# Performance work log

Measured on AMD Instinct MI355X. Metric: run time of the kernel, lower is better.

## Reference

```python
import jax, jax.numpy as jnp
import numpy as np

N_NODES = 100000
N_EDGES = 1600000
IN_DIM = 128
HID = 64


def _init_linear(key, fan_in, fan_out):
    kw, kb = jax.random.split(key)
    bound = 1.0 / np.sqrt(fan_in)
    W = jax.random.uniform(kw, (fan_in, fan_out), jnp.float32, -bound, bound)
    b = jax.random.uniform(kb, (fan_out,), jnp.float32, -bound, bound)
    return W, b


def setup_inputs() -> dict:
    key = jax.random.key(0)
    ks = jax.random.split(key, 6)
    x = jax.random.normal(ks[0], (N_NODES, IN_DIM), jnp.float32)
    edge_index = jax.random.randint(ks[1], (2, N_EDGES), 0, N_NODES, jnp.int64)
    W_pre, b_pre = _init_linear(ks[2], IN_DIM, HID)
    W1, b1 = _init_linear(ks[3], HID, HID)
    W2, b2 = _init_linear(ks[4], HID, HID)
    W3, b3 = _init_linear(ks[5], HID, HID)
    return {"x": x, "edge_index": edge_index, "W_pre": W_pre, "b_pre": b_pre,
            "W1": W1, "b1": b1, "W2": W2, "b2": b2, "W3": W3, "b3": b3}


def _gcn_layer(h, src, dst, dinv, W, b):
    # PyG GCNConv: h' = D^{-1/2} (A + I) D^{-1/2} (h W) + b, deg from A+I
    n = h.shape[0]
    hw = h @ W                                  # [N, out]
    norm = dinv[src] * dinv[dst]                # [E]
    msg = hw[src] * norm[:, None]               # gather + scale  [E, out]
    agg = jax.ops.segment_sum(msg, dst, num_segments=n)  # scatter-add
    agg = agg + hw * (dinv * dinv)[:, None]     # self-loop term (norm = dinv_i^2)
    return agg + b


def reference(x, edge_index, W_pre, b_pre, W1, b1, W2, b2, W3, b3):
    src, dst = edge_index[0], edge_index[1]
    n = x.shape[0]
    # degree of A + I (self loops added, as in GCNConv default)
    deg = jax.ops.segment_sum(jnp.ones(src.shape[0], x.dtype), dst, num_segments=n) + 1.0
    dinv = jax.lax.rsqrt(deg)

    h = x @ W_pre + b_pre                       # feature_pre linear
    h = jax.nn.relu(_gcn_layer(h, src, dst, dinv, W1, b1))  # dropout is identity in eval
    h = jax.nn.relu(_gcn_layer(h, src, dst, dinv, W2, b2))
    h = _gcn_layer(h, src, dst, dinv, W3, b3)
    # F.normalize(p=2, dim=-1) with eps=1e-12
    nrm = jnp.linalg.norm(h, axis=-1, keepdims=True)
    return h / jnp.maximum(nrm, 1e-12)
```

## Files before the change

kernel.cpp:

```cpp
#include <hip/hip_runtime.h>

#define N_NODES 100000
#define N_EDGES 1600000
#define IN_DIM 128
#define HID 64
#define NB 782
#define NBLK_GEMM 782
#define NGROUP 25000

typedef __attribute__((ext_vector_type(8))) _Float16 h8v;
typedef __attribute__((ext_vector_type(4))) float f4v;

struct Args {
  const float* x; const int* ei;
  const float* Wp; const float* bp;
  const float* W1; const float* b1;
  const float* W2; const float* b2;
  const float* W3; const float* b3;
  float* out;
  _Float16* bufA16; _Float16* hw16;
  int* pairs; int* csr; int* offs; float* dinv;
  int* bsz; int* bboff; int* bcur;
  _Float16* WpH; _Float16* WpL; _Float16* W1H; _Float16* W1L;
  _Float16* W2H; _Float16* W2L; _Float16* W3H; _Float16* W3L;
};

__device__ __forceinline__ void d_split(const float* __restrict__ W,
                                        _Float16* __restrict__ hi,
                                        _Float16* __restrict__ lo, int K, int i) {
  int k = i >> 6, n = i & 63;
  float v = W[i];
  _Float16 h = (_Float16)v;
  float r = v - (float)h;
  hi[n * K + k] = h;
  lo[n * K + k] = (_Float16)r;
}

__global__ __launch_bounds__(256) void f_prep(Args a) {
  int blk = blockIdx.x, t = threadIdx.x;
  if (blk < 32) d_split(a.Wp, a.WpH, a.WpL, IN_DIM, blk * 256 + t);
  else if (blk < 48) d_split(a.W1, a.W1H, a.W1L, HID, (blk - 32) * 256 + t);
  else if (blk < 64) d_split(a.W2, a.W2H, a.W2L, HID, (blk - 48) * 256 + t);
  else d_split(a.W3, a.W3H, a.W3L, HID, (blk - 64) * 256 + t);
}

__global__ __launch_bounds__(256) void f_bhist(Args a) {
  __shared__ int cnt[NB];
  int t = threadIdx.x;
  for (int i = t; i < NB; i += 256) cnt[i] = 0;
  __syncthreads();
  int e0 = blockIdx.x * 8192, e1 = min(e0 + 8192, N_EDGES);
  for (int e = e0 + t; e < e1; e += 256)
    atomicAdd(&cnt[a.ei[N_EDGES + e] >> 7], 1);
  __syncthreads();
  for (int i = t; i < NB; i += 256)
    if (cnt[i]) atomicAdd(&a.bsz[i], cnt[i]);
}

__global__ __launch_bounds__(256) void f_bscan(Args a) {
  __shared__ int sm[256];
  int t = threadIdx.x;
  int c[4];
  int idx0 = t * 4;
#pragma unroll
  for (int j = 0; j < 4; ++j) c[j] = (idx0 + j < NB) ? a.bsz[idx0 + j] : 0;
  int tsum = c[0] + c[1] + c[2] + c[3];
  int val = tsum;
  sm[t] = val;
  __syncthreads();
  for (int off = 1; off < 256; off <<= 1) {
    int u = (t >= off) ? sm[t - off] : 0;
    __syncthreads();
    val += u;
    sm[t] = val;
    __syncthreads();
  }
  int excl = val - tsum;
#pragma unroll
  for (int j = 0; j < 4; ++j) {
    int idx = idx0 + j;
    if (idx < NB) { a.bboff[idx] = excl; a.bcur[idx] = excl; }
    excl += c[j];
  }
  if (t == 255) a.bboff[NB] = val;
}

__global__ __launch_bounds__(256) void f_partition(Args a) {
  __shared__ int cnt[NB];
  __shared__ int base[NB];
  int t = threadIdx.x;
  for (int i = t; i < NB; i += 256) cnt[i] = 0;
  __syncthreads();
  int e0 = blockIdx.x * 8192, e1 = min(e0 + 8192, N_EDGES);
  for (int e = e0 + t; e < e1; e += 256)
    atomicAdd(&cnt[a.ei[N_EDGES + e] >> 7], 1);
  __syncthreads();
  for (int i = t; i < NB; i += 256) {
    int c = cnt[i];
    base[i] = c ? atomicAdd(&a.bcur[i], c) : 0;
    cnt[i] = 0;
  }
  __syncthreads();
  for (int e = e0 + t; e < e1; e += 256) {
    int s = a.ei[e];
    int d = a.ei[N_EDGES + e];
    int b = d >> 7;
    int r = atomicAdd(&cnt[b], 1);
    a.pairs[base[b] + r] = ((d & 127) << 17) | s;
  }
}

__global__ __launch_bounds__(256) void f_csrdeg(Args a) {
  __shared__ int ldeg[128];
  __shared__ int sc[128];
  __shared__ int lcur[128];
  int t = threadIdx.x;
  int b = blockIdx.x;
  int node0 = b << 7;
  int nloc = min(128, N_NODES - node0);
  int beg = a.bboff[b], end = a.bboff[b + 1];
  if (t < 128) ldeg[t] = 0;
  __syncthreads();
  for (int i = beg + t; i < end; i += 256)
    atomicAdd(&ldeg[(a.pairs[i] >> 17) & 127], 1);
  __syncthreads();
  int dv = (t < 128) ? ldeg[t] : 0;
  if (t < 128) sc[t] = dv;
  __syncthreads();
  for (int off = 1; off < 128; off <<= 1) {
    int u = (t >= off && t < 128) ? sc[t - off] : 0;
    __syncthreads();
    if (t < 128) sc[t] += u;
    __syncthreads();
  }
  if (t < nloc) {
    int o = beg + sc[t] - dv;
    a.offs[node0 + t] = o;
    lcur[t] = o;
    a.dinv[node0 + t] = rsqrtf((float)dv + 1.0f);
  }
  if (b == NB - 1 && t == 0) a.offs[N_NODES] = N_EDGES;
  __syncthreads();
  for (int i = beg + t; i < end; i += 256) {
    int p = a.pairs[i];
    int pos = atomicAdd(&lcur[(p >> 17) & 127], 1);
    a.csr[pos] = p & 131071;
  }
}

__global__ __launch_bounds__(256) void f_gemm_pre(Args a) {
  __shared__ _Float16 sW[2 * 64 * IN_DIM];
  int t = threadIdx.x;
  int wave = t >> 6, lane = t & 63, fi = lane & 15, quad = lane >> 4;
  int r0 = blockIdx.x * 128 + wave * 32;

  f4v xb0[8], xb1[8];
  {
    int row = r0 + fi; if (row >= N_NODES) row = N_NODES - 1;
    const float* xp = a.x + (size_t)row * IN_DIM + quad * 8;
#pragma unroll
    for (int j = 0; j < 4; ++j) {
      xb0[2 * j]     = *(const f4v*)(xp + j * 32);
      xb0[2 * j + 1] = *(const f4v*)(xp + j * 32 + 4);
    }
  }
#pragma unroll
  for (int i = 0; i < 8; ++i) {
    int c = i * 256 + t;
    int h = c >> 10;
    int c2 = c & 1023;
    int n = c2 >> 4;
    const _Float16* src = (h ? a.WpL : a.WpH) + c2 * 8;
    f4v v = *(const f4v*)src;
    int off = (h << 14) | ((c2 * 16) ^ ((n & 7) << 4));
    *(f4v*)((char*)sW + off) = v;
  }
  __syncthreads();

  float bv[4];
#pragma unroll
  for (int ct = 0; ct < 4; ++ct) bv[ct] = a.bp[ct * 16 + fi];

#pragma unroll
  for (int f = 0; f < 2; ++f) {
    f4v* xcur = (f & 1) ? xb1 : xb0;
    f4v* xnxt = (f & 1) ? xb0 : xb1;
    if (f < 1) {
      int row = r0 + 16 + fi; if (row >= N_NODES) row = N_NODES - 1;
      const float* xp = a.x + (size_t)row * IN_DIM + quad * 8;
#pragma unroll
      for (int j = 0; j < 4; ++j) {
        xnxt[2 * j]     = *(const f4v*)(xp + j * 32);
        xnxt[2 * j + 1] = *(const f4v*)(xp + j * 32 + 4);
      }
    }
    f4v acc[4];
#pragma unroll
    for (int ct = 0; ct < 4; ++ct) acc[ct] = (f4v){0.f, 0.f, 0.f, 0.f};
#pragma unroll
    for (int k0i = 0; k0i < 4; ++k0i) {
      h8v ah, al;
#pragma unroll
      for (int j = 0; j < 4; ++j) {
        float v0 = xcur[2 * k0i][j], v1 = xcur[2 * k0i + 1][j];
        _Float16 h0 = (_Float16)v0, h1 = (_Float16)v1;
        ah[j] = h0;     al[j] = (_Float16)(v0 - (float)h0);
        ah[4 + j] = h1; al[4 + j] = (_Float16)(v1 - (float)h1);
      }
#pragma unroll
      for (int ct = 0; ct < 4; ++ct) {
        int n = ct * 16 + fi;
        int bo = ((n * IN_DIM + k0i * 32 + quad * 8) * 2) ^ ((n & 7) << 4);
        h8v bh = *(const h8v*)((const char*)sW + bo);
        h8v bl = *(const h8v*)((const char*)sW + 16384 + bo);
        acc[ct] = __builtin_amdgcn_mfma_f32_16x16x32_f16(ah, bh, acc[ct], 0, 0, 0);
        acc[ct] = __builtin_amdgcn_mfma_f32_16x16x32_f16(al, bh, acc[ct], 0, 0, 0);
        acc[ct] = __builtin_amdgcn_mfma_f32_16x16x32_f16(ah, bl, acc[ct], 0, 0, 0);
      }
    }
    int ro = r0 + f * 16;
#pragma unroll
    for (int ct = 0; ct < 4; ++ct) {
#pragma unroll
      for (int j = 0; j < 4; ++j) {
        int orow = ro + quad * 4 + j;
        if (orow < N_NODES)
          a.bufA16[(size_t)orow * HID + ct * 16 + fi] = (_Float16)(acc[ct][j] + bv[ct]);
      }
    }
  }
}

__global__ __launch_bounds__(256) void f_gemm64(Args a, const _Float16* __restrict__ Wh,
                                                const _Float16* __restrict__ Wl) {
  int t = threadIdx.x;
  int wave = t >> 6, lane = t & 63, fi = lane & 15, quad = lane >> 4;
  int r0 = blockIdx.x * 128 + wave * 32;

  h8v a0[2], a1[2];
  {
    int row = r0 + fi; if (row >= N_NODES) row = N_NODES - 1;
    const _Float16* xp = a.bufA16 + (size_t)row * HID + quad * 8;
    a0[0] = *(const h8v*)xp;
    a0[1] = *(const h8v*)(xp + 32);
  }
  h8v Bh[2][4], Bl[2][4];
#pragma unroll
  for (int k0i = 0; k0i < 2; ++k0i)
#pragma unroll
    for (int ct = 0; ct < 4; ++ct) {
      size_t o = (size_t)(ct * 16 + fi) * HID + k0i * 32 + quad * 8;
      Bh[k0i][ct] = *(const h8v*)(Wh + o);
      Bl[k0i][ct] = *(const h8v*)(Wl + o);
    }

#pragma unroll
  for (int f = 0; f < 2; ++f) {
    h8v* av = (f & 1) ? a1 : a0;
    h8v* nx = (f & 1) ? a0 : a1;
    if (f < 1) {
      int row = r0 + 16 + fi; if (row >= N_NODES) row = N_NODES - 1;
      const _Float16* xp = a.bufA16 + (size_t)row * HID + quad * 8;
      nx[0] = *(const h8v*)xp;
      nx[1] = *(const h8v*)(xp + 32);
    }
    f4v acc[4];
#pragma unroll
    for (int ct = 0; ct < 4; ++ct) acc[ct] = (f4v){0.f, 0.f, 0.f, 0.f};
#pragma unroll
    for (int k0i = 0; k0i < 2; ++k0i)
#pragma unroll
      for (int ct = 0; ct < 4; ++ct) {
        acc[ct] = __builtin_amdgcn_mfma_f32_16x16x32_f16(av[k0i], Bh[k0i][ct], acc[ct], 0, 0, 0);
        acc[ct] = __builtin_amdgcn_mfma_f32_16x16x32_f16(av[k0i], Bl[k0i][ct], acc[ct], 0, 0, 0);
      }
    int ro = r0 + f * 16;
#pragma unroll
    for (int ct = 0; ct < 4; ++ct)
#pragma unroll
      for (int j = 0; j < 4; ++j) {
        int orow = ro + quad * 4 + j;
        if (orow < N_NODES)
          a.hw16[(size_t)orow * HID + ct * 16 + fi] = (_Float16)acc[ct][j];
      }
  }
}

template <int MODE>
__device__ __forceinline__ void d_agg(int grp, const _Float16* __restrict__ hw,
                                      const int* __restrict__ offs,
                                      const int* __restrict__ csr,
                                      const float* __restrict__ dinv,
                                      const float* __restrict__ bias,
                                      _Float16* __restrict__ out16,
                                      float* __restrict__ out32) {
  int node = grp * 4 + (threadIdx.x >> 6);
  int lane = threadIdx.x & 63;
  int oct = lane >> 3;
  int fi = lane & 7;
  float di = dinv[node];
  int beg = offs[node];
  int end = offs[node + 1];

  float acc[8];
#pragma unroll
  for (int c = 0; c < 8; ++c) acc[c] = 0.f;

  if (oct == 0) {
    h8v hv = *(const h8v*)(hw + (size_t)node * HID + fi * 8);
    float w = di * di;
#pragma unroll
    for (int c = 0; c < 8; ++c) acc[c] += (float)hv[c] * w;
  }
  for (int e0 = beg + oct; e0 < end; e0 += 32) {
    int ss[4];
    float ww[4];
#pragma unroll
    for (int j = 0; j < 4; ++j) {
      int e = e0 + 8 * j;
      bool v = e < end;
      int s = csr[v ? e : beg];
      ss[j] = v ? s : node;
      ww[j] = v ? di : 0.0f;
    }
#pragma unroll
    for (int j = 0; j < 4; ++j) ww[j] *= dinv[ss[j]];
    h8v hv[4];
#pragma unroll
    for (int j = 0; j < 4; ++j)
      hv[j] = *(const h8v*)(hw + (size_t)ss[j] * HID + fi * 8);
#pragma unroll
    for (int j = 0; j < 4; ++j)
#pragma unroll
      for (int c = 0; c < 8; ++c) acc[c] += (float)hv[j][c] * ww[j];
  }
#pragma unroll
  for (int c = 0; c < 8; ++c) {
    float v = acc[c];
    v += __shfl_xor(v, 8);
    v += __shfl_xor(v, 16);
    v += __shfl_xor(v, 32);
    acc[c] = v;
  }
  if (oct == 0) {
#pragma unroll
    for (int c = 0; c < 8; ++c) acc[c] += bias[fi * 8 + c];
    if (MODE == 0) {
      h8v o;
#pragma unroll
      for (int c = 0; c < 8; ++c) o[c] = (_Float16)fmaxf(acc[c], 0.f);
      *(h8v*)(out16 + (size_t)node * HID + fi * 8) = o;
    } else {
      float ss = 0.f;
#pragma unroll
      for (int c = 0; c < 8; ++c) ss += acc[c] * acc[c];
      ss += __shfl_xor(ss, 1);
      ss += __shfl_xor(ss, 2);
      ss += __shfl_xor(ss, 4);
      float sc = 1.0f / fmaxf(sqrtf(ss), 1e-12f);
      f4v o0 = {acc[0] * sc, acc[1] * sc, acc[2] * sc, acc[3] * sc};
      f4v o1 = {acc[4] * sc, acc[5] * sc, acc[6] * sc, acc[7] * sc};
      *(f4v*)(out32 + (size_t)node * HID + fi * 8) = o0;
      *(f4v*)(out32 + (size_t)node * HID + fi * 8 + 4) = o1;
    }
  }
}

__global__ __launch_bounds__(256) void f_agg_relu(Args a, const float* bias) {
  d_agg<0>(blockIdx.x, a.hw16, a.offs, a.csr, a.dinv, bias, a.bufA16, nullptr);
}

__global__ __launch_bounds__(256) void f_agg_norm(Args a) {
  d_agg<1>(blockIdx.x, a.hw16, a.offs, a.csr, a.dinv, a.b3, nullptr, a.out);
}

extern "C" void kernel_launch(void* const* d_in, const int* in_sizes, int n_in,
                              void* d_out, int out_size, void* d_ws, size_t ws_size,
                              hipStream_t stream) {
  char* ws = (char*)d_ws;
  Args a;
  a.x  = (const float*)d_in[0];
  a.ei = (const int*)d_in[1];
  a.Wp = (const float*)d_in[2];  a.bp = (const float*)d_in[3];
  a.W1 = (const float*)d_in[4];  a.b1 = (const float*)d_in[5];
  a.W2 = (const float*)d_in[6];  a.b2 = (const float*)d_in[7];
  a.W3 = (const float*)d_in[8];  a.b3 = (const float*)d_in[9];
  a.out  = (float*)d_out;
  a.bufA16 = (_Float16*)(ws + 0);
  a.hw16   = (_Float16*)(ws + 12800000);
  a.pairs  = (int*)(ws + 25600000);
  a.csr    = (int*)(ws + 32000000);
  a.offs   = (int*)(ws + 38400000);
  a.dinv   = (float*)(ws + 38800016);
  a.bsz    = (int*)(ws + 39200016);
  a.bboff  = (int*)(ws + 39203152);
  a.bcur   = (int*)(ws + 39206288);
  a.WpH = (_Float16*)(ws + 39210000);
  a.WpL = (_Float16*)(ws + 39226384);
  a.W1H = (_Float16*)(ws + 39242768);
  a.W1L = (_Float16*)(ws + 39250960);
  a.W2H = (_Float16*)(ws + 39259152);
  a.W2L = (_Float16*)(ws + 39267344);
  a.W3H = (_Float16*)(ws + 39275536);
  a.W3L = (_Float16*)(ws + 39283728);

  (void)hipMemsetAsync(a.bsz, 0, NB * sizeof(int), stream);
  f_prep<<<80, 256, 0, stream>>>(a);
  f_bhist<<<196, 256, 0, stream>>>(a);
  f_bscan<<<1, 256, 0, stream>>>(a);
  f_partition<<<196, 256, 0, stream>>>(a);
  f_csrdeg<<<NB, 256, 0, stream>>>(a);
  f_gemm_pre<<<NBLK_GEMM, 256, 0, stream>>>(a);
  f_gemm64<<<NBLK_GEMM, 256, 0, stream>>>(a, a.W1H, a.W1L);
  f_agg_relu<<<NGROUP, 256, 0, stream>>>(a, a.b1);
  f_gemm64<<<NBLK_GEMM, 256, 0, stream>>>(a, a.W2H, a.W2L);
  f_agg_relu<<<NGROUP, 256, 0, stream>>>(a, a.b2);
  f_gemm64<<<NBLK_GEMM, 256, 0, stream>>>(a, a.W3H, a.W3L);
  f_agg_norm<<<NGROUP, 256, 0, stream>>>(a);
}
```

Measured before the change: 347.3 us.

## Restructure GCN aggregation to one feature per lane with readlane-broadcast neighbors

Replaces the 8-octet-by-8-feature aggregation (each octet handles separate edges with 16-byte fp16 vector loads, then a cross-octet shuffle reduction) with a scheme where each lane owns one feature. Edge indices and weights are loaded cooperatively 64 at a time and broadcast with readlane, so every lane gathers one fp16 element per neighbor. This removes the final shuffle reduction and the idle-octet writeback, but switches from 16-byte to 2-byte per-lane gather loads and serializes the edges of each node across iterations.

```diff
diff --git a/kernel.cpp b/kernel.cpp
--- a/kernel.cpp
+++ b/kernel.cpp
@@ -296,73 +296,46 @@
                                       float* __restrict__ out32) {
   int node = grp * 4 + (threadIdx.x >> 6);
   int lane = threadIdx.x & 63;
-  int oct = lane >> 3;
-  int fi = lane & 7;
   float di = dinv[node];
   int beg = offs[node];
   int end = offs[node + 1];
-
-  float acc[8];
-#pragma unroll
-  for (int c = 0; c < 8; ++c) acc[c] = 0.f;
-
-  if (oct == 0) {
-    h8v hv = *(const h8v*)(hw + (size_t)node * HID + fi * 8);
-    float w = di * di;
-#pragma unroll
-    for (int c = 0; c < 8; ++c) acc[c] += (float)hv[c] * w;
-  }
-  for (int e0 = beg + oct; e0 < end; e0 += 32) {
-    int ss[4];
-    float ww[4];
-#pragma unroll
-    for (int j = 0; j < 4; ++j) {
-      int e = e0 + 8 * j;
-      bool v = e < end;
-      int s = csr[v ? e : beg];
-      ss[j] = v ? s : node;
-      ww[j] = v ? di : 0.0f;
-    }
-#pragma unroll
-    for (int j = 0; j < 4; ++j) ww[j] *= dinv[ss[j]];
-    h8v hv[4];
-#pragma unroll
-    for (int j = 0; j < 4; ++j)
-      hv[j] = *(const h8v*)(hw + (size_t)ss[j] * HID + fi * 8);
-#pragma unroll
-    for (int j = 0; j < 4; ++j)
-#pragma unroll
-      for (int c = 0; c < 8; ++c) acc[c] += (float)hv[j][c] * ww[j];
-  }
-#pragma unroll
-  for (int c = 0; c < 8; ++c) {
-    float v = acc[c];
-    v += __shfl_xor(v, 8);
-    v += __shfl_xor(v, 16);
-    v += __shfl_xor(v, 32);
-    acc[c] = v;
-  }
-  if (oct == 0) {
-#pragma unroll
-    for (int c = 0; c < 8; ++c) acc[c] += bias[fi * 8 + c];
-    if (MODE == 0) {
-      h8v o;
-#pragma unroll
-      for (int c = 0; c < 8; ++c) o[c] = (_Float16)fmaxf(acc[c], 0.f);
-      *(h8v*)(out16 + (size_t)node * HID + fi * 8) = o;
-    } else {
-      float ss = 0.f;
-#pragma unroll
-      for (int c = 0; c < 8; ++c) ss += acc[c] * acc[c];
-      ss += __shfl_xor(ss, 1);
-      ss += __shfl_xor(ss, 2);
-      ss += __shfl_xor(ss, 4);
-      float sc = 1.0f / fmaxf(sqrtf(ss), 1e-12f);
-      f4v o0 = {acc[0] * sc, acc[1] * sc, acc[2] * sc, acc[3] * sc};
-      f4v o1 = {acc[4] * sc, acc[5] * sc, acc[6] * sc, acc[7] * sc};
-      *(f4v*)(out32 + (size_t)node * HID + fi * 8) = o0;
-      *(f4v*)(out32 + (size_t)node * HID + fi * 8 + 4) = o1;
-    }
+  int deg = end - beg;
+  float bv = bias[lane];
+
+  _Float16 hself = hw[(size_t)node * HID + lane];
+  float acc = (float)hself * (di * di);
+
+  for (int c0 = 0; c0 < deg; c0 += 64) {
+    int nc = min(64, deg - c0);
+    int ei = beg + c0 + ((lane < nc) ? lane : (nc - 1));
+    int sv = csr[ei];
+    float wv = (lane < nc) ? dinv[sv] * di : 0.0f;
+
+    int rn = (nc + 7) & ~7;
+    for (int j = 0; j < rn; j += 8) {
+      _Float16 v[8];
+      float wj[8];
+#pragma unroll
+      for (int u = 0; u < 8; ++u) {
+        int sj = __builtin_amdgcn_readlane(sv, j + u);
+        wj[u] = __int_as_float(__builtin_amdgcn_readlane(__float_as_int(wv), j + u));
+        const _Float16* p = hw + ((size_t)sj << 6);
+        v[u] = p[lane];
+      }
+#pragma unroll
+      for (int u = 0; u < 8; ++u) acc += (float)v[u] * wj[u];
+    }
+  }
+
+  acc += bv;
+  if (MODE == 0) {
+    out16[(size_t)node * HID + lane] = (_Float16)fmaxf(acc, 0.f);
+  } else {
+    float ss = acc * acc;
+#pragma unroll
+    for (int w = 1; w < 64; w <<= 1) ss += __shfl_xor(ss, w);
+    float sc = 1.0f / fmaxf(sqrtf(ss), 1e-12f);
+    out32[(size_t)node * HID + lane] = acc * sc;
   }
 }
 
```

Measured after the change: 358.8 us. 1.03x slower.

## Pre-scale CSR indices to byte offsets and use fused fp16-mix FMAs in aggregation

Applied to the files above, without the earlier changes.

Stores CSR source entries as byte offsets (node<<7) so the gather address needs no multiply, and factors the destination dinv out of the per-edge weight, applying it once after reduction. The per-edge fp16-to-fp32 convert plus FMA is replaced by inline v_fma_mix_f32. The unroll drops from 4 to 2 edges per iteration, which exposes less memory-level parallelism per lane. Storing node<<7 in int limits node ids to about 16M, which is fine here.

```diff
diff --git a/kernel.cpp b/kernel.cpp
--- a/kernel.cpp
+++ b/kernel.cpp
@@ -25,6 +25,15 @@
   _Float16* W2H; _Float16* W2L; _Float16* W3H; _Float16* W3L;
 };
 
+__device__ __forceinline__ void fmix_lo(float& acc, unsigned hv, float w) {
+  asm("v_fma_mix_f32 %0, %1, %2, %0 op_sel:[0,0,0] op_sel_hi:[1,0,0]"
+      : "+v"(acc) : "v"(hv), "v"(w));
+}
+__device__ __forceinline__ void fmix_hi(float& acc, unsigned hv, float w) {
+  asm("v_fma_mix_f32 %0, %1, %2, %0 op_sel:[1,0,0] op_sel_hi:[1,0,0]"
+      : "+v"(acc) : "v"(hv), "v"(w));
+}
+
 __device__ __forceinline__ void d_split(const float* __restrict__ W,
                                         _Float16* __restrict__ hi,
                                         _Float16* __restrict__ lo, int K, int i) {
@@ -144,7 +153,7 @@
   for (int i = beg + t; i < end; i += 256) {
     int p = a.pairs[i];
     int pos = atomicAdd(&lcur[(p >> 17) & 127], 1);
-    a.csr[pos] = p & 131071;
+    a.csr[pos] = (p & 131071) << 7;
   }
 }
 
@@ -301,38 +310,37 @@
   float di = dinv[node];
   int beg = offs[node];
   int end = offs[node + 1];
+  int lb = fi * 16;
+  const char* hwb = (const char*)hw;
 
   float acc[8];
 #pragma unroll
   for (int c = 0; c < 8; ++c) acc[c] = 0.f;
 
   if (oct == 0) {
-    h8v hv = *(const h8v*)(hw + (size_t)node * HID + fi * 8);
-    float w = di * di;
-#pragma unroll
-    for (int c = 0; c < 8; ++c) acc[c] += (float)hv[c] * w;
-  }
-  for (int e0 = beg + oct; e0 < end; e0 += 32) {
-    int ss[4];
-    float ww[4];
-#pragma unroll
-    for (int j = 0; j < 4; ++j) {
-      int e = e0 + 8 * j;
-      bool v = e < end;
-      int s = csr[v ? e : beg];
-      ss[j] = v ? s : node;
-      ww[j] = v ? di : 0.0f;
-    }
-#pragma unroll
-    for (int j = 0; j < 4; ++j) ww[j] *= dinv[ss[j]];
-    h8v hv[4];
-#pragma unroll
-    for (int j = 0; j < 4; ++j)
-      hv[j] = *(const h8v*)(hw + (size_t)ss[j] * HID + fi * 8);
-#pragma unroll
-    for (int j = 0; j < 4; ++j)
-#pragma unroll
-      for (int c = 0; c < 8; ++c) acc[c] += (float)hv[j][c] * ww[j];
+    uint4 hv = *(const uint4*)(hwb + ((size_t)node << 7) + lb);
+    fmix_lo(acc[0], hv.x, di); fmix_hi(acc[1], hv.x, di);
+    fmix_lo(acc[2], hv.y, di); fmix_hi(acc[3], hv.y, di);
+    fmix_lo(acc[4], hv.z, di); fmix_hi(acc[5], hv.z, di);
+    fmix_lo(acc[6], hv.w, di); fmix_hi(acc[7], hv.w, di);
+  }
+  for (int e0 = beg + oct; e0 < end; e0 += 16) {
+    int off0 = csr[e0];
+    int e1 = e0 + 8;
+    bool v1 = e1 < end;
+    int off1 = csr[v1 ? e1 : beg];
+    float w0 = dinv[(unsigned)off0 >> 7];
+    float w1 = v1 ? dinv[(unsigned)off1 >> 7] : 0.0f;
+    uint4 h0 = *(const uint4*)(hwb + (unsigned)off0 + lb);
+    uint4 h1 = *(const uint4*)(hwb + (unsigned)off1 + lb);
+    fmix_lo(acc[0], h0.x, w0); fmix_hi(acc[1], h0.x, w0);
+    fmix_lo(acc[2], h0.y, w0); fmix_hi(acc[3], h0.y, w0);
+    fmix_lo(acc[4], h0.z, w0); fmix_hi(acc[5], h0.z, w0);
+    fmix_lo(acc[6], h0.w, w0); fmix_hi(acc[7], h0.w, w0);
+    fmix_lo(acc[0], h1.x, w1); fmix_hi(acc[1], h1.x, w1);
+    fmix_lo(acc[2], h1.y, w1); fmix_hi(acc[3], h1.y, w1);
+    fmix_lo(acc[4], h1.z, w1); fmix_hi(acc[5], h1.z, w1);
+    fmix_lo(acc[6], h1.w, w1); fmix_hi(acc[7], h1.w, w1);
   }
 #pragma unroll
   for (int c = 0; c < 8; ++c) {
@@ -344,7 +352,7 @@
   }
   if (oct == 0) {
 #pragma unroll
-    for (int c = 0; c < 8; ++c) acc[c] += bias[fi * 8 + c];
+    for (int c = 0; c < 8; ++c) acc[c] = acc[c] * di + bias[fi * 8 + c];
     if (MODE == 0) {
       h8v o;
 #pragma unroll
```

Result: slower. 361.3 us (+4.0%).
